# Kernel tuning notes

Measured on AMD Instinct MI355X. Metric: run time of the kernel, lower is better.

Reference implementation:

```python
import jax, jax.numpy as jnp
import numpy as np

N = 100000      # nodes
E = 1600000     # edges (avg degree 16)
D = 64          # node feature dim
MSG = 2 * D     # message dim = concat(src, dst)
HID = MSG + D   # hidden dim = concat(message_sum, h_n)
ALPHA = 0.01    # LeakyReLU slope


def leaky_relu(x):
    return jnp.where(x >= 0, x, ALPHA * x)


def setup_inputs() -> dict:
    key = jax.random.key(0)
    ks = jax.random.split(key, 7)
    h_n = jax.random.normal(ks[0], (N, D), dtype=jnp.float32)
    src = jax.random.randint(ks[1], (E,), 0, N)
    dst = jax.random.randint(ks[2], (E,), 0, N)
    Wm = jax.random.normal(ks[3], (MSG, MSG), dtype=jnp.float32) / np.sqrt(MSG).astype(np.float32)
    bm = jax.random.normal(ks[4], (MSG,), dtype=jnp.float32) * 0.01
    Wh = jax.random.normal(ks[5], (HID, HID), dtype=jnp.float32) / np.sqrt(HID).astype(np.float32)
    bh = jax.random.normal(ks[6], (HID,), dtype=jnp.float32) * 0.01
    return {"h_n": h_n, "src": src, "dst": dst, "Wm": Wm, "bm": bm, "Wh": Wh, "bh": bh}


def reference(h_n, src, dst, Wm, bm, Wh, bh):
    # Message function: per-edge gather + concat + linear + activation.
    msg_in = jnp.concatenate([h_n[src], h_n[dst]], axis=-1)        # [E, 2D]
    msg = leaky_relu(msg_in @ Wm.T + bm)                            # [E, MSG]
    # fn.sum('message', 'message_sum'): scatter-sum to destination nodes.
    msg_sum = jax.ops.segment_sum(msg, dst, num_segments=N)        # [N, MSG]
    # Node update: concat + linear + activation.
    hid_in = jnp.concatenate([msg_sum, h_n], axis=-1)              # [N, MSG+D]
    h_out = leaky_relu(hid_in @ Wh.T + bh)                          # [N, HID]
    # unique-id split/squeeze is an identity when all node ids are unique.
    return h_out
```

## Files before the change

### kernel.cpp

```cpp
#include <hip/hip_runtime.h>

#define FD 64
#define MSGD 128
#define HIDD 192
#define ALPHA 0.01f
#define SCAN_CHUNK 1024

typedef __attribute__((ext_vector_type(8))) short short8;
typedef __attribute__((ext_vector_type(4))) float f32x4;
typedef unsigned int uint32;

__device__ __forceinline__ float leaky(float x) { return x >= 0.0f ? x : ALPHA * x; }

__device__ __forceinline__ uint32 f2b(float x) {
    uint32 u = __builtin_bit_cast(uint32, x);
    return (u + 0x7fffu + ((u >> 16) & 1u)) >> 16;
}
__device__ __forceinline__ uint32 pk(float lo, float hi) { return f2b(lo) | (f2b(hi) << 16); }
__device__ __forceinline__ float b2f(uint32 lo16) { return __builtin_bit_cast(float, lo16 << 16); }

__global__ __launch_bounds__(256) void conv_kernel(
    const float* __restrict__ h, const float* __restrict__ Wh, const float* __restrict__ Wm,
    uint32* __restrict__ hidb32 , uint32* __restrict__ whb32 ,
    uint32* __restrict__ wmb32 , int N)
{
    int u = blockIdx.x * 256 + threadIdx.x;
    const int HUNITS = N * 8;
    const int WHUNITS = HIDD * HIDD / 8;
    const int WMUNITS = MSGD * MSGD / 8;
    if (u < HUNITS) {
        int row = u >> 3, g = u & 7;
        const float4* s = reinterpret_cast<const float4*>(h + (size_t)row * FD + g * 8);
        float4 v0 = s[0], v1 = s[1];
        uint32* d = hidb32 + (size_t)row * 96 + 64 + g * 4;
        d[0] = pk(v0.x, v0.y); d[1] = pk(v0.z, v0.w);
        d[2] = pk(v1.x, v1.y); d[3] = pk(v1.z, v1.w);
    } else if (u < HUNITS + WHUNITS) {
        int idx = (u - HUNITS) * 8;
        const float4* s = reinterpret_cast<const float4*>(Wh + idx);
        float4 v0 = s[0], v1 = s[1];
        uint32* d = whb32 + (idx >> 1);
        d[0] = pk(v0.x, v0.y); d[1] = pk(v0.z, v0.w);
        d[2] = pk(v1.x, v1.y); d[3] = pk(v1.z, v1.w);
    } else if (u < HUNITS + WHUNITS + WMUNITS) {
        int idx = (u - HUNITS - WHUNITS) * 8;
        const float4* s = reinterpret_cast<const float4*>(Wm + idx);
        float4 v0 = s[0], v1 = s[1];
        uint32* d = wmb32 + (idx >> 1);
        d[0] = pk(v0.x, v0.y); d[1] = pk(v0.z, v0.w);
        d[2] = pk(v1.x, v1.y); d[3] = pk(v1.z, v1.w);
    }
}

__global__ __launch_bounds__(256) void ab_mfma_kernel(
    const short* __restrict__ hidb,
    const short* __restrict__ wmb,
    const float* __restrict__ bm,
    uint32* __restrict__ Abf, uint32* __restrict__ Bbf, int N)
{
    const int t = threadIdx.x, l = t & 63, q = t >> 6;
    const int node0 = blockIdx.x * 64 + q * 16;
    const int lg = l >> 4, lm = l & 15;

    const int brow = min(node0 + lm, N - 1);
    const short* hp = hidb + (size_t)brow * HIDD + 128 + lg * 8;
    const short8 b0 = *reinterpret_cast<const short8*>(hp);
    const short8 b1 = *reinterpret_cast<const short8*>(hp + 32);

    const int node = node0 + lm;
    const bool nv = (node < N);

    #pragma unroll
    for (int jt = 0; jt < 8; ++jt) {
        const int jrow = jt * 16 + lg * 4;
        {
            const short* wp = wmb + (size_t)(jt * 16 + lm) * MSGD + lg * 8;
            f32x4 c = {0.0f, 0.0f, 0.0f, 0.0f};
            c = __builtin_amdgcn_mfma_f32_16x16x32_bf16(
                    *reinterpret_cast<const short8*>(wp), b0, c, 0, 0, 0);
            c = __builtin_amdgcn_mfma_f32_16x16x32_bf16(
                    *reinterpret_cast<const short8*>(wp + 32), b1, c, 0, 0, 0);
            if (nv) {
                uint32* pa = Abf + (size_t)node * 64 + (jrow >> 1);
                pa[0] = pk(c[0], c[1]);
                pa[1] = pk(c[2], c[3]);
            }
        }
        {
            const short* wp = wmb + (size_t)(jt * 16 + lm) * MSGD + 64 + lg * 8;
            f32x4 c = {0.0f, 0.0f, 0.0f, 0.0f};
            c = __builtin_amdgcn_mfma_f32_16x16x32_bf16(
                    *reinterpret_cast<const short8*>(wp), b0, c, 0, 0, 0);
            c = __builtin_amdgcn_mfma_f32_16x16x32_bf16(
                    *reinterpret_cast<const short8*>(wp + 32), b1, c, 0, 0, 0);
            if (nv) {
                uint32* pb = Bbf + (size_t)node * 64 + (jrow >> 1);
                pb[0] = pk(c[0] + bm[jrow + 0], c[1] + bm[jrow + 1]);
                pb[1] = pk(c[2] + bm[jrow + 2], c[3] + bm[jrow + 3]);
            }
        }
    }
}

__global__ void count_kernel(const int* __restrict__ dst, int* __restrict__ rowstart, int E) {
    int e = blockIdx.x * 256 + threadIdx.x;
    if (e < E) atomicAdd(&rowstart[dst[e] + 1], 1);
}

__global__ __launch_bounds__(256) void scan_chunk_kernel(
    int* __restrict__ data, int* __restrict__ partials, int len)
{
    __shared__ int sums[2][256];
    const int t = threadIdx.x;
    const int base = blockIdx.x * SCAN_CHUNK + t * 4;
    int v[4];
    #pragma unroll
    for (int i = 0; i < 4; ++i) v[i] = (base + i < len) ? data[base + i] : 0;
    v[1] += v[0]; v[2] += v[1]; v[3] += v[2];
    sums[0][t] = v[3];
    __syncthreads();
    int pp = 0;
    for (int off = 1; off < 256; off <<= 1) {
        int val = sums[pp][t];
        if (t >= off) val += sums[pp][t - off];
        sums[pp ^ 1][t] = val;
        pp ^= 1;
        __syncthreads();
    }
    int prefix = (t > 0) ? sums[pp][t - 1] : 0;
    #pragma unroll
    for (int i = 0; i < 4; ++i) if (base + i < len) data[base + i] = v[i] + prefix;
    if (t == 255) partials[blockIdx.x] = sums[pp][255];
}

__global__ __launch_bounds__(128) void scan_top_kernel(int* __restrict__ partials, int nchunks) {
    __shared__ int sums[2][128];
    const int t = threadIdx.x;
    sums[0][t] = (t < nchunks) ? partials[t] : 0;
    __syncthreads();
    int pp = 0;
    for (int off = 1; off < 128; off <<= 1) {
        int val = sums[pp][t];
        if (t >= off) val += sums[pp][t - off];
        sums[pp ^ 1][t] = val;
        pp ^= 1;
        __syncthreads();
    }
    if (t < nchunks) partials[t] = sums[pp][t];
}

__global__ __launch_bounds__(256) void scan_add_kernel(
    int* __restrict__ data, const int* __restrict__ partials, int len)
{
    const int c = blockIdx.x + 1;
    const int base = c * SCAN_CHUNK + threadIdx.x * 4;
    const int add = partials[c - 1];
    #pragma unroll
    for (int i = 0; i < 4; ++i) if (base + i < len) data[base + i] += add;
}

__global__ void scatter_kernel(const int* __restrict__ src, const int* __restrict__ dst,
                               const int* __restrict__ rowstart, int* __restrict__ cursor,
                               int* __restrict__ csr_src, int E)
{
    int e = blockIdx.x * 256 + threadIdx.x;
    if (e < E) {
        int d = dst[e];
        int pos = rowstart[d] + atomicAdd(&cursor[d], 1);
        csr_src[pos] = src[e];
    }
}

__global__ __launch_bounds__(256) void gather_kernel(
    const uint32* __restrict__ Abf, const uint32* __restrict__ Bbf,
    uint32* __restrict__ hidb32, const int* __restrict__ csr_src,
    const int* __restrict__ rowstart, int N)
{
    const int w = (int)((blockIdx.x * (size_t)blockDim.x + threadIdx.x) >> 6);
    const int lane = threadIdx.x & 63;
    if (w >= N) return;
    const int p0 = rowstart[w], p1 = rowstart[w + 1];
    const uint32 bpkd = Bbf[(size_t)w * 64 + lane];
    const float b0 = b2f(bpkd & 0xffffu), b1 = b2f(bpkd >> 16);
    float acc0 = 0.0f, acc1 = 0.0f;
    int p = p0;
    for (; p + 4 <= p1; p += 4) {
        int s0 = __builtin_amdgcn_readfirstlane(csr_src[p]);
        int s1 = __builtin_amdgcn_readfirstlane(csr_src[p + 1]);
        int s2 = __builtin_amdgcn_readfirstlane(csr_src[p + 2]);
        int s3 = __builtin_amdgcn_readfirstlane(csr_src[p + 3]);
        uint32 a0 = Abf[(size_t)s0 * 64 + lane];
        uint32 a1 = Abf[(size_t)s1 * 64 + lane];
        uint32 a2 = Abf[(size_t)s2 * 64 + lane];
        uint32 a3 = Abf[(size_t)s3 * 64 + lane];
        acc0 += leaky(b2f(a0 & 0xffffu) + b0); acc1 += leaky(b2f(a0 >> 16) + b1);
        acc0 += leaky(b2f(a1 & 0xffffu) + b0); acc1 += leaky(b2f(a1 >> 16) + b1);
        acc0 += leaky(b2f(a2 & 0xffffu) + b0); acc1 += leaky(b2f(a2 >> 16) + b1);
        acc0 += leaky(b2f(a3 & 0xffffu) + b0); acc1 += leaky(b2f(a3 >> 16) + b1);
    }
    for (; p < p1; ++p) {
        int s0 = __builtin_amdgcn_readfirstlane(csr_src[p]);
        uint32 a0 = Abf[(size_t)s0 * 64 + lane];
        acc0 += leaky(b2f(a0 & 0xffffu) + b0);
        acc1 += leaky(b2f(a0 >> 16) + b1);
    }
    hidb32[(size_t)w * 96 + lane] = pk(acc0, acc1);
}

__global__ __launch_bounds__(256) void node_mfma_kernel(
    const short* __restrict__ hidb, const short* __restrict__ whb,
    const float* __restrict__ bh, float* __restrict__ out, int N)
{
    const int t = threadIdx.x, l = t & 63, q = t >> 6;
    const int mbase = blockIdx.x * 64 + q * 16;
    const int lg = l >> 4, lm = l & 15;

    const int arow = min(mbase + lm, N - 1);
    const short* ap = hidb + (size_t)arow * HIDD + lg * 8;
    short8 a[6];
    #pragma unroll
    for (int kc = 0; kc < 6; ++kc)
        a[kc] = *reinterpret_cast<const short8*>(ap + kc * 32);

    f32x4 acc[12];
    const short* bp0 = whb + (size_t)lm * HIDD + lg * 8;
    #pragma unroll
    for (int nt = 0; nt < 12; ++nt) {
        const short* bp = bp0 + (size_t)nt * 16 * HIDD;
        f32x4 c = {0.0f, 0.0f, 0.0f, 0.0f};
        #pragma unroll
        for (int kc = 0; kc < 6; ++kc) {
            short8 b = *reinterpret_cast<const short8*>(bp + kc * 32);
            c = __builtin_amdgcn_mfma_f32_16x16x32_bf16(a[kc], b, c, 0, 0, 0);
        }
        acc[nt] = c;
    }

    const int orow0 = mbase + lg * 4;
    #pragma unroll
    for (int nt = 0; nt < 12; ++nt) {
        const int col = nt * 16 + lm;
        const float bias = bh[col];
        #pragma unroll
        for (int r = 0; r < 4; ++r) {
            const int row = orow0 + r;
            if (row < N) out[(size_t)row * HIDD + col] = leaky(acc[nt][r] + bias);
        }
    }
}

__global__ __launch_bounds__(256, 2) void edge_kernel(
    const float* __restrict__ h, const int* __restrict__ src, const int* __restrict__ dst,
    const float* __restrict__ Wm, const float* __restrict__ bm,
    float* __restrict__ msg_sum, int E)
{
    __shared__ float in_t[MSGD][64];
    const int t = threadIdx.x, le = t & 63, q = t >> 6;
    const int e = blockIdx.x * 64 + le;
    const bool ev = (e < E);
    int node = 0;
    if (ev) node = (q < 2) ? src[e] : dst[e];
    const float4* row = reinterpret_cast<const float4*>(h + (size_t)node * FD + (q & 1) * 32);
    #pragma unroll
    for (int i = 0; i < 8; ++i) {
        float4 v = row[i];
        int k = q * 32 + i * 4;
        in_t[k+0][le] = v.x; in_t[k+1][le] = v.y; in_t[k+2][le] = v.z; in_t[k+3][le] = v.w;
    }
    __syncthreads();
    const int jbase = __builtin_amdgcn_readfirstlane(q) * 32;
    float acc[32];
    #pragma unroll
    for (int jj = 0; jj < 32; ++jj) acc[jj] = bm[jbase + jj];
    #pragma unroll 1
    for (int kc = 0; kc < 4; ++kc) {
        float inr[32];
        #pragma unroll
        for (int i = 0; i < 32; ++i) inr[i] = in_t[kc * 32 + i][le];
        #pragma unroll
        for (int jj = 0; jj < 32; ++jj) {
            const float* wrow = Wm + (size_t)(jbase + jj) * MSGD + kc * 32;
            #pragma unroll
            for (int i = 0; i < 32; ++i) acc[jj] = fmaf(inr[i], wrow[i], acc[jj]);
        }
    }
    if (ev) {
        float* outp = msg_sum + (size_t)dst[e] * MSGD + jbase;
        #pragma unroll
        for (int jj = 0; jj < 32; ++jj) unsafeAtomicAdd(outp + jj, leaky(acc[jj]));
    }
}

__global__ __launch_bounds__(256, 2) void node_kernel(
    const float* __restrict__ h, const float* __restrict__ msg_sum,
    const float* __restrict__ Wh, const float* __restrict__ bh,
    float* __restrict__ out, int N)
{
    __shared__ float in_t[HIDD][64];
    const int t = threadIdx.x, ln = t & 63, q = t >> 6;
    const int n = blockIdx.x * 64 + ln;
    const bool nv = (n < N);
    const int nn = nv ? n : 0;
    {
        const float4* row = reinterpret_cast<const float4*>(msg_sum + (size_t)nn * MSGD + q * 32);
        #pragma unroll
        for (int i = 0; i < 8; ++i) {
            float4 v = row[i];
            int k = q * 32 + i * 4;
            in_t[k+0][ln] = v.x; in_t[k+1][ln] = v.y; in_t[k+2][ln] = v.z; in_t[k+3][ln] = v.w;
        }
        const float4* row2 = reinterpret_cast<const float4*>(h + (size_t)nn * FD + q * 16);
        #pragma unroll
        for (int i = 0; i < 4; ++i) {
            float4 v = row2[i];
            int k = MSGD + q * 16 + i * 4;
            in_t[k+0][ln] = v.x; in_t[k+1][ln] = v.y; in_t[k+2][ln] = v.z; in_t[k+3][ln] = v.w;
        }
    }
    __syncthreads();
    const int jbase = __builtin_amdgcn_readfirstlane(q) * 48;
    float acc[48];
    #pragma unroll
    for (int jj = 0; jj < 48; ++jj) acc[jj] = bh[jbase + jj];
    #pragma unroll 1
    for (int kc = 0; kc < 6; ++kc) {
        float inr[32];
        #pragma unroll
        for (int i = 0; i < 32; ++i) inr[i] = in_t[kc * 32 + i][ln];
        #pragma unroll
        for (int jj = 0; jj < 48; ++jj) {
            const float* wrow = Wh + (size_t)(jbase + jj) * HIDD + kc * 32;
            #pragma unroll
            for (int i = 0; i < 32; ++i) acc[jj] = fmaf(inr[i], wrow[i], acc[jj]);
        }
    }
    if (nv) {
        float* op = out + (size_t)n * HIDD + jbase;
        #pragma unroll
        for (int i = 0; i < 12; ++i) {
            float4 v;
            v.x = leaky(acc[i*4+0]); v.y = leaky(acc[i*4+1]);
            v.z = leaky(acc[i*4+2]); v.w = leaky(acc[i*4+3]);
            reinterpret_cast<float4*>(op)[i] = v;
        }
    }
}

extern "C" void kernel_launch(void* const* d_in, const int* in_sizes, int n_in,
                              void* d_out, int out_size, void* d_ws, size_t ws_size,
                              hipStream_t stream) {
    const float* h   = (const float*)d_in[0];
    const int*   src = (const int*)  d_in[1];
    const int*   dst = (const int*)  d_in[2];
    const float* Wm  = (const float*)d_in[3];
    const float* bm  = (const float*)d_in[4];
    const float* Wh  = (const float*)d_in[5];
    const float* bh  = (const float*)d_in[6];
    float* out = (float*)d_out;

    const int N = in_sizes[0] / FD;
    const int E = in_sizes[1];

    uint32* Abf    = (uint32*)d_ws;
    uint32* Bbf    = Abf + (size_t)N * 64;
    uint32* hidb32 = Bbf + (size_t)N * 64;
    uint32* whb32  = hidb32 + (size_t)N * 96;
    uint32* wmb32  = whb32 + (HIDD * HIDD / 2);
    int* csr_src   = (int*)(wmb32 + (MSGD * MSGD / 2));
    int* rowstart  = csr_src + E;
    int* cursor    = rowstart + (N + 1);
    const int nchunks = (N + SCAN_CHUNK - 1) / SCAN_CHUNK;
    int* partials  = cursor + N;

    const size_t need = ((size_t)N * (64 + 64 + 96) + (HIDD * HIDD / 2) + (MSGD * MSGD / 2)
                        + (size_t)E + 2 * (size_t)N + 1 + 512) * sizeof(int);

    if (ws_size >= need && nchunks <= 128) {
        hipMemsetAsync(rowstart, 0, (2 * (size_t)N + 1 + 512) * sizeof(int), stream);
        const int UNITS = N * 8 + (HIDD * HIDD / 8) + (MSGD * MSGD / 8);
        conv_kernel<<<(UNITS + 255) / 256, 256, 0, stream>>>(
            h, Wh, Wm, hidb32, whb32, wmb32, N);
        ab_mfma_kernel<<<(N + 63) / 64, 256, 0, stream>>>(
            (const short*)hidb32, (const short*)wmb32, bm, Abf, Bbf, N);
        count_kernel<<<(E + 255) / 256, 256, 0, stream>>>(dst, rowstart, E);
        scan_chunk_kernel<<<nchunks, 256, 0, stream>>>(rowstart + 1, partials, N);
        scan_top_kernel<<<1, 128, 0, stream>>>(partials, nchunks);
        if (nchunks > 1)
            scan_add_kernel<<<nchunks - 1, 256, 0, stream>>>(rowstart + 1, partials, N);
        scatter_kernel<<<(E + 255) / 256, 256, 0, stream>>>(src, dst, rowstart, cursor, csr_src, E);
        gather_kernel<<<(int)(((size_t)N * 64 + 255) / 256), 256, 0, stream>>>(
            Abf, Bbf, hidb32, csr_src, rowstart, N);
        node_mfma_kernel<<<(N + 63) / 64, 256, 0, stream>>>(
            (const short*)hidb32, (const short*)whb32, bh, out, N);
    } else {
        float* msg_sum = (float*)d_ws;
        hipMemsetAsync(msg_sum, 0, (size_t)N * MSGD * sizeof(float), stream);
        edge_kernel<<<(E + 63) / 64, 256, 0, stream>>>(h, src, dst, Wm, bm, msg_sum, E);
        node_kernel<<<(N + 63) / 64, 256, 0, stream>>>(h, msg_sum, Wh, bh, out, N);
    }
}
```

Before: 453.0 us.

## Record atomic rank in count pass, drop scatter atomics; double node MFMA tile

The count kernel now stores the value returned by each edge's atomic increment as that edge's rank. The placement kernel then writes csr_src at rowstart+rank with no second atomic pass, and the cursor array and its memset go away. This costs an extra E-sized rank array that is written and read back. Separately, node_mfma_kernel now handles 32 rows per wave (128 per block), reusing each loaded Wh fragment for two MFMAs and storing each tile right after computing it, which raises register use.

```diff
diff --git a/kernel.cpp b/kernel.cpp
--- a/kernel.cpp
+++ b/kernel.cpp
@@ -102,9 +102,10 @@
     }
 }
 
-__global__ void count_kernel(const int* __restrict__ dst, int* __restrict__ rowstart, int E) {
+__global__ void count_kernel(const int* __restrict__ dst, int* __restrict__ rowstart,
+                             int* __restrict__ rank, int E) {
     int e = blockIdx.x * 256 + threadIdx.x;
-    if (e < E) atomicAdd(&rowstart[dst[e] + 1], 1);
+    if (e < E) rank[e] = atomicAdd(&rowstart[dst[e] + 1], 1);
 }
 
 __global__ __launch_bounds__(256) void scan_chunk_kernel(
@@ -159,16 +160,12 @@
     for (int i = 0; i < 4; ++i) if (base + i < len) data[base + i] += add;
 }
 
-__global__ void scatter_kernel(const int* __restrict__ src, const int* __restrict__ dst,
-                               const int* __restrict__ rowstart, int* __restrict__ cursor,
-                               int* __restrict__ csr_src, int E)
+__global__ void place_kernel(const int* __restrict__ src, const int* __restrict__ dst,
+                             const int* __restrict__ rowstart, const int* __restrict__ rank,
+                             int* __restrict__ csr_src, int E)
 {
     int e = blockIdx.x * 256 + threadIdx.x;
-    if (e < E) {
-        int d = dst[e];
-        int pos = rowstart[d] + atomicAdd(&cursor[d], 1);
-        csr_src[pos] = src[e];
-    }
+    if (e < E) csr_src[rowstart[dst[e]] + rank[e]] = src[e];
 }
 
 __global__ __launch_bounds__(256) void gather_kernel(
@@ -212,39 +209,40 @@
     const float* __restrict__ bh, float* __restrict__ out, int N)
 {
     const int t = threadIdx.x, l = t & 63, q = t >> 6;
-    const int mbase = blockIdx.x * 64 + q * 16;
+    const int mbase = blockIdx.x * 128 + q * 32;
     const int lg = l >> 4, lm = l & 15;
 
-    const int arow = min(mbase + lm, N - 1);
-    const short* ap = hidb + (size_t)arow * HIDD + lg * 8;
-    short8 a[6];
-    #pragma unroll
-    for (int kc = 0; kc < 6; ++kc)
-        a[kc] = *reinterpret_cast<const short8*>(ap + kc * 32);
-
-    f32x4 acc[12];
+    const int ar0 = min(mbase + lm, N - 1);
+    const int ar1 = min(mbase + 16 + lm, N - 1);
+    const short* ap0 = hidb + (size_t)ar0 * HIDD + lg * 8;
+    const short* ap1 = hidb + (size_t)ar1 * HIDD + lg * 8;
+    short8 a0[6], a1[6];
+    #pragma unroll
+    for (int kc = 0; kc < 6; ++kc) {
+        a0[kc] = *reinterpret_cast<const short8*>(ap0 + kc * 32);
+        a1[kc] = *reinterpret_cast<const short8*>(ap1 + kc * 32);
+    }
+
     const short* bp0 = whb + (size_t)lm * HIDD + lg * 8;
+    const int r0 = mbase + lg * 4;
     #pragma unroll
     for (int nt = 0; nt < 12; ++nt) {
         const short* bp = bp0 + (size_t)nt * 16 * HIDD;
-        f32x4 c = {0.0f, 0.0f, 0.0f, 0.0f};
+        f32x4 c0 = {0.0f, 0.0f, 0.0f, 0.0f};
+        f32x4 c1 = {0.0f, 0.0f, 0.0f, 0.0f};
         #pragma unroll
         for (int kc = 0; kc < 6; ++kc) {
             short8 b = *reinterpret_cast<const short8*>(bp + kc * 32);
-            c = __builtin_amdgcn_mfma_f32_16x16x32_bf16(a[kc], b, c, 0, 0, 0);
-        }
-        acc[nt] = c;
-    }
-
-    const int orow0 = mbase + lg * 4;
-    #pragma unroll
-    for (int nt = 0; nt < 12; ++nt) {
+            c0 = __builtin_amdgcn_mfma_f32_16x16x32_bf16(a0[kc], b, c0, 0, 0, 0);
+            c1 = __builtin_amdgcn_mfma_f32_16x16x32_bf16(a1[kc], b, c1, 0, 0, 0);
+        }
         const int col = nt * 16 + lm;
         const float bias = bh[col];
         #pragma unroll
         for (int r = 0; r < 4; ++r) {
-            const int row = orow0 + r;
-            if (row < N) out[(size_t)row * HIDD + col] = leaky(acc[nt][r] + bias);
+            const int row0 = r0 + r, row1 = r0 + 16 + r;
+            if (row0 < N) out[(size_t)row0 * HIDD + col] = leaky(c0[r] + bias);
+            if (row1 < N) out[(size_t)row1 * HIDD + col] = leaky(c1[r] + bias);
         }
     }
 }
@@ -367,30 +365,30 @@
     uint32* whb32  = hidb32 + (size_t)N * 96;
     uint32* wmb32  = whb32 + (HIDD * HIDD / 2);
     int* csr_src   = (int*)(wmb32 + (MSGD * MSGD / 2));
-    int* rowstart  = csr_src + E;
-    int* cursor    = rowstart + (N + 1);
+    int* rank      = csr_src + E;
+    int* rowstart  = rank + E;
+    int* partials  = rowstart + (N + 1);
     const int nchunks = (N + SCAN_CHUNK - 1) / SCAN_CHUNK;
-    int* partials  = cursor + N;
 
     const size_t need = ((size_t)N * (64 + 64 + 96) + (HIDD * HIDD / 2) + (MSGD * MSGD / 2)
-                        + (size_t)E + 2 * (size_t)N + 1 + 512) * sizeof(int);
+                        + 2 * (size_t)E + (size_t)N + 1 + 512) * sizeof(int);
 
     if (ws_size >= need && nchunks <= 128) {
-        hipMemsetAsync(rowstart, 0, (2 * (size_t)N + 1 + 512) * sizeof(int), stream);
+        hipMemsetAsync(rowstart, 0, ((size_t)N + 1 + 512) * sizeof(int), stream);
         const int UNITS = N * 8 + (HIDD * HIDD / 8) + (MSGD * MSGD / 8);
         conv_kernel<<<(UNITS + 255) / 256, 256, 0, stream>>>(
             h, Wh, Wm, hidb32, whb32, wmb32, N);
         ab_mfma_kernel<<<(N + 63) / 64, 256, 0, stream>>>(
             (const short*)hidb32, (const short*)wmb32, bm, Abf, Bbf, N);
-        count_kernel<<<(E + 255) / 256, 256, 0, stream>>>(dst, rowstart, E);
+        count_kernel<<<(E + 255) / 256, 256, 0, stream>>>(dst, rowstart, rank, E);
         scan_chunk_kernel<<<nchunks, 256, 0, stream>>>(rowstart + 1, partials, N);
         scan_top_kernel<<<1, 128, 0, stream>>>(partials, nchunks);
         if (nchunks > 1)
             scan_add_kernel<<<nchunks - 1, 256, 0, stream>>>(rowstart + 1, partials, N);
-        scatter_kernel<<<(E + 255) / 256, 256, 0, stream>>>(src, dst, rowstart, cursor, csr_src, E);
+        place_kernel<<<(E + 255) / 256, 256, 0, stream>>>(src, dst, rowstart, rank, csr_src, E);
         gather_kernel<<<(int)(((size_t)N * 64 + 255) / 256), 256, 0, stream>>>(
             Abf, Bbf, hidb32, csr_src, rowstart, N);
-        node_mfma_kernel<<<(N + 63) / 64, 256, 0, stream>>>(
+        node_mfma_kernel<<<(N + 127) / 128, 256, 0, stream>>>(
             (const short*)hidb32, (const short*)whb32, bh, out, N);
     } else {
         float* msg_sum = (float*)d_ws;
```

After: 375.9 us. -17.0%, faster.
